# Kernel optimization log

Measured on AMD Instinct MI355X. Metric: run time of the kernel, lower is better.

Reference implementation:

```python
import jax, jax.numpy as jnp
import numpy as np

N, LQ, DM = 8, 2500, 256
NH, NL, NP, NZ = 8, 4, 8, 4
DH = DM // NH
SPATIAL = np.array([[64, 176], [32, 88], [16, 44], [8, 22]], dtype=np.int32)
LEN_IN = int((SPATIAL[:, 0] * SPATIAL[:, 1]).sum())


def setup_inputs() -> dict:
    key = jax.random.key(0)
    ks = jax.random.split(key, 10)
    query = jax.random.normal(ks[0], (N, LQ, DM), dtype=jnp.float32)
    query_pos = jax.random.normal(ks[1], (N, LQ, DM), dtype=jnp.float32)
    reference_points = jax.random.uniform(ks[2], (N, LQ, NZ, 2), dtype=jnp.float32)
    input_flatten = jax.random.normal(ks[3], (N, LEN_IN, DM), dtype=jnp.float32)
    input_spatial_shapes = jnp.asarray(SPATIAL)
    lsi = np.concatenate([[0], np.cumsum(SPATIAL[:, 0] * SPATIAL[:, 1])[:-1]]).astype(np.int32)
    input_level_start_index = jnp.asarray(lsi)
    # learned params (Linear: y = x @ W + b, W is (in, out))
    Wv = jax.random.normal(ks[4], (DM, DM), dtype=jnp.float32) * (1.0 / np.sqrt(DM))
    bv = jnp.zeros((DM,), dtype=jnp.float32)
    Wo = jax.random.normal(ks[5], (DM, NH * NL * NP * 2), dtype=jnp.float32) * 0.02
    bo = jax.random.normal(ks[6], (NH * NL * NP * 2,), dtype=jnp.float32) * 1.0
    Wa = jax.random.normal(ks[7], (DM, NH * NL * NP), dtype=jnp.float32) * 0.02
    ba = jnp.zeros((NH * NL * NP,), dtype=jnp.float32)
    return {"query": query, "query_pos": query_pos, "reference_points": reference_points,
            "input_flatten": input_flatten, "input_spatial_shapes": input_spatial_shapes,
            "input_level_start_index": input_level_start_index,
            "Wv": Wv, "bv": bv, "Wo": Wo, "bo": bo, "Wa": Wa, "ba": ba}


def _sample_level(v, h, w, loc):
    """Bilinear sample (grid_sample, align_corners=False, zero padding).
    v:   (N, h*w, NH, DH) level feature map
    loc: (N, Lq, NH, P, 2) normalized locations in [0,1] (x, y)
    returns (N, NH, Lq, P, DH)
    """
    n, hw, nh, dh = v.shape
    lq, p = loc.shape[1], loc.shape[3]
    x = loc[..., 0] * w - 0.5
    y = loc[..., 1] * h - 0.5
    x0f = jnp.floor(x)
    y0f = jnp.floor(y)
    wx = x - x0f
    wy = y - y0f
    x0 = x0f.astype(jnp.int32)
    y0 = y0f.astype(jnp.int32)
    vt = v.transpose(0, 2, 1, 3).reshape(n * nh, hw, dh)

    def gather(xi, yi, wgt):
        valid = ((xi >= 0) & (xi < w) & (yi >= 0) & (yi < h)).astype(v.dtype)
        idx = jnp.clip(yi, 0, h - 1) * w + jnp.clip(xi, 0, w - 1)  # (N,Lq,NH,P)
        idx = idx.transpose(0, 2, 1, 3).reshape(n * nh, lq * p)
        g = jnp.take_along_axis(vt, idx[:, :, None], axis=1)  # (N*NH, Lq*P, DH)
        wv = (wgt * valid).transpose(0, 2, 1, 3).reshape(n * nh, lq * p)
        return g * wv[:, :, None]

    out = (gather(x0, y0, (1 - wx) * (1 - wy))
           + gather(x0 + 1, y0, wx * (1 - wy))
           + gather(x0, y0 + 1, (1 - wx) * wy)
           + gather(x0 + 1, y0 + 1, wx * wy))
    return out.reshape(n, nh, lq, p, dh)


def _forward(query, query_pos, reference_points, input_flatten, spatial, Wv, bv, Wo, bo, Wa, ba):
    n, lq, _ = query.shape
    len_in = input_flatten.shape[1]
    # projections
    value = (input_flatten @ Wv + bv).reshape(n, len_in, NH, DH)
    off = (query @ Wo + bo).reshape(n, lq, NH, NL, NP, 2)
    aw = jax.nn.softmax((query @ Wa + ba).reshape(n, lq, NH, NL * NP), axis=-1)
    aw = aw.reshape(n, lq, NH, NL, NP)
    # normalize offsets by (W_l, H_l), add to Z-anchor reference points
    norm = jnp.asarray(np.stack([spatial[:, 1], spatial[:, 0]], -1), dtype=query.dtype)  # (NL,2)
    off = off / norm[None, None, None, :, None, :]
    off = off.reshape(n, lq, NH, NL, NP // NZ, NZ, 2)
    ref = reference_points[:, :, None, None, None, :, :]  # (N,Lq,1,1,1,NZ,2)
    loc = (ref + off).reshape(n, lq, NH, NL, NP, 2)
    # multi-scale deformable sampling + weighted reduction
    out = jnp.zeros((n, lq, NH, DH), dtype=query.dtype)
    start = 0
    for lvl in range(NL):
        h, w = int(spatial[lvl, 0]), int(spatial[lvl, 1])
        v_l = value[:, start:start + h * w]
        start += h * w
        samp = _sample_level(v_l, h, w, loc[:, :, :, lvl])  # (N,NH,Lq,NP,DH)
        out = out + jnp.einsum('nhqpd,nqhp->nqhd', samp, aw[:, :, :, lvl])
    return out.reshape(n, lq, DM)


def reference(query, query_pos, reference_points, input_flatten, input_spatial_shapes,
              input_level_start_index, Wv, bv, Wo, bo, Wa, ba):
    spatial = np.asarray(jax.device_get(input_spatial_shapes))
    return _forward(query, query_pos, reference_points, input_flatten, spatial,
                    Wv, bv, Wo, bo, Wa, ba)
```

## Files before the change

### kernel.cpp

```cpp
#include <hip/hip_runtime.h>
#include <hip/hip_fp16.h>

#define N_BATCH 8
#define LQ_     2500
#define DM_     256
#define NH_     8
#define NL_     4
#define NP_     8
#define DH_     32
#define LEN_IN_ 14960
#define KDIM    256

#define MV_   119680
#define MQ_   20000
#define NBMV  935
#define NBMQ  157
#define NVB   1872
#define NCB   960

__constant__ int c_w[4]     = {176, 88, 44, 22};
__constant__ int c_h[4]     = {64, 32, 16, 8};
__constant__ int c_start[4] = {0, 11264, 14080, 14784};

using bf16x8 = __attribute__((ext_vector_type(8))) short;
using f32x4  = __attribute__((ext_vector_type(4))) float;

#define GLDS16(g, l)                                                         \
    __builtin_amdgcn_global_load_lds(                                        \
        (const __attribute__((address_space(1))) void*)(g),                  \
        (__attribute__((address_space(3))) void*)(l), 16, 0, 0)

static __device__ inline float fdot2_u(unsigned int p, unsigned int w, float c) {
    float r;
    asm("v_dot2_f32_f16 %0, %1, %2, %3" : "=v"(r) : "v"(p), "v"(w), "v"(c));
    return r;
}

static __device__ inline void split_bf16(float v, unsigned short& hi, unsigned short& lo) {
    unsigned int u = __float_as_uint(v);
    hi = (unsigned short)(u >> 16);
    float hif = __uint_as_float(u & 0xFFFF0000u);
    float l = v - hif;
    lo = (unsigned short)(__float_as_uint(l) >> 16);
}

static __device__ inline unsigned short f2bf_rne(float v) {
    unsigned int u = __float_as_uint(v);
    u += 0x7FFFu + ((u >> 16) & 1u);
    return (unsigned short)(u >> 16);
}

static __device__ inline unsigned short f2h_rne(float v) {
    _Float16 h = (_Float16)v;
    return __builtin_bit_cast(unsigned short, h);
}

static __device__ inline ushort4 cvt4_rne(float4 v) {
    ushort4 h;
    h.x = f2bf_rne(v.x);
    h.y = f2bf_rne(v.y);
    h.z = f2bf_rne(v.z);
    h.w = f2bf_rne(v.w);
    return h;
}

__global__ __launch_bounds__(256) void prep(
    const float* __restrict__ Wv, const float* __restrict__ Wo,
    const float* __restrict__ Wa, const float* __restrict__ bo,
    const float* __restrict__ ba,
    const float* __restrict__ input_flatten, const float* __restrict__ query,
    unsigned short* __restrict__ Wv_hi, unsigned short* __restrict__ Wv_lo,
    unsigned short* __restrict__ Wc_hi, unsigned short* __restrict__ Wc_lo,
    float* __restrict__ bcomb,
    unsigned short* __restrict__ Abf_v, unsigned short* __restrict__ Abf_q)
{
    const int b = blockIdx.x, tid = threadIdx.x;
    if (b < 2048) {
        const float4* s = (const float4*)input_flatten;
        ushort4*      d = (ushort4*)Abf_v;
        const int n8 = MV_ * KDIM / 8, st = 2048 * 256;
        for (int i = b * 256 + tid; i < n8; i += st) {
            d[2 * i]     = cvt4_rne(s[2 * i]);
            d[2 * i + 1] = cvt4_rne(s[2 * i + 1]);
        }
    } else if (b < 2560) {
        const float4* s = (const float4*)query;
        ushort4*      d = (ushort4*)Abf_q;
        const int n8 = MQ_ * KDIM / 8, st = 512 * 256;
        for (int i = (b - 2048) * 256 + tid; i < n8; i += st) {
            d[2 * i]     = cvt4_rne(s[2 * i]);
            d[2 * i + 1] = cvt4_rne(s[2 * i + 1]);
        }
    } else {
        const int base = (b - 2560) * 256 + tid;
        for (int id = base; id < 262144; id += 131072) {
            if (id < 65536) {
                int n = id >> 8, k = id & 255;
                unsigned short h, l;
                split_bf16(Wv[k * 256 + n], h, l);
                Wv_hi[id] = h; Wv_lo[id] = l;
            } else {
                int id2 = id - 65536;
                int n = id2 >> 8, k = id2 & 255;
                float v = (n < 512) ? Wo[k * 512 + n] : Wa[k * 256 + (n - 512)];
                unsigned short h, l;
                split_bf16(v, h, l);
                Wc_hi[id2] = h; Wc_lo[id2] = l;
            }
        }
        if (base < 768) bcomb[base] = (base < 512) ? bo[base] : ba[base - 512];
    }
}

__global__ __launch_bounds__(512, 8) void gemm2(
    const unsigned short* __restrict__ Av,
    const unsigned short* __restrict__ Aq,
    const unsigned short* __restrict__ Wvh, const unsigned short* __restrict__ Wvl,
    const unsigned short* __restrict__ Wch, const unsigned short* __restrict__ Wcl,
    const float* __restrict__ bv, const float* __restrict__ bc,
    float* __restrict__ Cq,
    unsigned short* __restrict__ Cv)
{
    __shared__ __align__(16) unsigned short As [4096];
    __shared__ __align__(16) unsigned short Bhs[4096];
    __shared__ __align__(16) unsigned short Bls[4096];

    const int tid = threadIdx.x;
    const int bid = blockIdx.x;
    const bool is_comb = (bid >= NVB);

    const unsigned short *A, *Bth, *Btl;
    const float* bias;
    int by, bx, M, N;
    if (is_comb) {
        int cid = bid - NVB;
        int xcd = cid & 7, j = cid >> 3;
        by = xcd + 8 * (j / 6); bx = j % 6;
        if (by >= NBMQ) return;
        A = Aq; Bth = Wch; Btl = Wcl; bias = bc;
        M = MQ_; N = 768;
    } else {
        int xcd = bid & 7, j = bid >> 3;
        by = xcd + 8 * (j >> 1); bx = j & 1;
        if (by >= NBMV) return;
        A = Av; Bth = Wvh; Btl = Wvl; bias = bv;
        M = MV_; N = 256;
    }

    const int row0 = by << 7, col0 = bx << 7;
    const int lane = tid & 63, wave = tid >> 6;
    const int wrow = (wave & 1) << 6, wcol = (wave >> 1) << 5;
    const int r16  = lane & 15, quad = lane >> 4;

    const int srow = tid >> 2, skq = tid & 3;
    const int arow = min(row0 + srow, M - 1);
    const unsigned short* gA  = A   + (size_t)arow * KDIM + skq * 8;
    const unsigned short* gBh = Bth + (size_t)(col0 + srow) * KDIM + skq * 8;
    const unsigned short* gBl = Btl + (size_t)(col0 + srow) * KDIM + skq * 8;
    unsigned short* lA  = &As [wave << 9];
    unsigned short* lBh = &Bhs[wave << 9];
    unsigned short* lBl = &Bls[wave << 9];

    f32x4 acc[4][2];
#pragma unroll
    for (int i = 0; i < 4; ++i)
#pragma unroll
        for (int j = 0; j < 2; ++j) acc[i][j] = (f32x4){0.f, 0.f, 0.f, 0.f};

#pragma unroll
    for (int kt = 0; kt < 8; ++kt) {
        GLDS16(gA  + kt * 32, lA);
        GLDS16(gBh + kt * 32, lBh);
        GLDS16(gBl + kt * 32, lBl);
        __syncthreads();

        bf16x8 fbh[2], fbl[2], fa[4];
#pragma unroll
        for (int tn = 0; tn < 2; ++tn) {
            int n = wcol + tn * 16 + r16;
            fbh[tn] = *(const bf16x8*)&Bhs[n * 32 + (quad << 3)];
            fbl[tn] = *(const bf16x8*)&Bls[n * 32 + (quad << 3)];
        }
#pragma unroll
        for (int tm = 0; tm < 4; ++tm)
            fa[tm] = *(const bf16x8*)&As[(wrow + tm * 16 + r16) * 32 + (quad << 3)];
#pragma unroll
        for (int tm = 0; tm < 4; ++tm)
#pragma unroll
            for (int tn = 0; tn < 2; ++tn) {
                acc[tm][tn] = __builtin_amdgcn_mfma_f32_16x16x32_bf16(fa[tm], fbl[tn], acc[tm][tn], 0, 0, 0);
                acc[tm][tn] = __builtin_amdgcn_mfma_f32_16x16x32_bf16(fa[tm], fbh[tn], acc[tm][tn], 0, 0, 0);
            }
        __syncthreads();
    }

    float bvs[2];
#pragma unroll
    for (int tn = 0; tn < 2; ++tn) bvs[tn] = bias[col0 + wcol + tn * 16 + r16];
#pragma unroll
    for (int tm = 0; tm < 4; ++tm) {
#pragma unroll
        for (int i = 0; i < 4; ++i) {
            int row = row0 + wrow + tm * 16 + (quad << 2) + i;
            if (row < M) {
                if (is_comb) {
                    float* crow = Cq + (size_t)row * N + col0 + wcol + r16;
#pragma unroll
                    for (int tn = 0; tn < 2; ++tn)
                        crow[tn * 16] = acc[tm][tn][i] + bvs[tn];
                } else {
                    int n   = row / LEN_IN_;
                    int pix = row - n * LEN_IN_;
#pragma unroll
                    for (int tn = 0; tn < 2; ++tn) {
                        int col = col0 + wcol + tn * 16 + r16;
                        int h = col >> 5, dh = col & 31;
                        size_t addr = ((size_t)(n * NH_ + h) * LEN_IN_ + pix) * DH_ + dh;
                        Cv[addr] = f2h_rne(acc[tm][tn][i] + bvs[tn]);
                    }
                }
            }
        }
    }
}

__global__ __launch_bounds__(256, 4) void ms_sample(
    const unsigned short* __restrict__ value,
    const float* __restrict__ comb,
    const float* __restrict__ ref_pts,
    float* __restrict__ out)
{
    __shared__ uint4 s_desc[64][33];

    const int b     = blockIdx.x;
    const int xcd   = b & 7;
    const int j     = b >> 3;
    const int slice = (j / 40) * 8 + xcd;
    const int chunk = j % 40;
    const int n     = slice >> 3, h = slice & 7;
    const int q0    = chunk * 64;
    const int tid   = threadIdx.x;

    {
        int ql = tid >> 2, l = tid & 3;
        int q  = q0 + ql;
        if (q < LQ_) {
            int nq = n * LQ_ + q;
            const float* row = comb + (size_t)nq * 768;

            float4 L0 = *(const float4*)&row[512 + h * 32 + l * 8];
            float4 L1 = *(const float4*)&row[512 + h * 32 + l * 8 + 4];
            float lg[8] = {L0.x, L0.y, L0.z, L0.w, L1.x, L1.y, L1.z, L1.w};
            float m = lg[0];
#pragma unroll
            for (int i = 1; i < 8; ++i) m = fmaxf(m, lg[i]);
            m = fmaxf(m, __shfl_xor(m, 1));
            m = fmaxf(m, __shfl_xor(m, 2));
            float e[8], s = 0.f;
#pragma unroll
            for (int i = 0; i < 8; ++i) { e[i] = __expf(lg[i] - m); s += e[i]; }
            s += __shfl_xor(s, 1);
            s += __shfl_xor(s, 2);
            float inv = 1.f / s;

            float4 R0 = *(const float4*)&ref_pts[(size_t)nq * 8];
            float4 R1 = *(const float4*)&ref_pts[(size_t)nq * 8 + 4];
            float rx[4] = {R0.x, R0.z, R1.x, R1.z};
            float ry[4] = {R0.y, R0.w, R1.y, R1.w};

            float off[16];
#pragma unroll
            for (int i = 0; i < 4; ++i)
                *(float4*)&off[i * 4] = *(const float4*)&row[h * 64 + l * 16 + i * 4];

            float wl = (float)c_w[l], hl = (float)c_h[l];
            int wli = c_w[l], hli = c_h[l], st = c_start[l];
#pragma unroll
            for (int p = 0; p < 8; ++p) {
                int z = p & 3;
                float a = e[p] * inv;
                float x = rx[z] * wl + off[p * 2 + 0] - 0.5f;
                float y = ry[z] * hl + off[p * 2 + 1] - 0.5f;
                float x0f = floorf(x), y0f = floorf(y);
                int   x0 = (int)x0f,  y0 = (int)y0f;
                float wx = x - x0f,   wy = y - y0f;
                unsigned short ix[4];
                float wt[4];
#pragma unroll
                for (int jj = 0; jj < 4; ++jj) {
                    int xi = x0 + (jj & 1);
                    int yi = y0 + (jj >> 1);
                    float w = ((jj & 1) ? wx : 1.f - wx) * ((jj >> 1) ? wy : 1.f - wy);
                    bool valid = (xi >= 0) && (xi < wli) && (yi >= 0) && (yi < hli);
                    int xc = min(max(xi, 0), wli - 1);
                    int yc = min(max(yi, 0), hli - 1);
                    ix[jj] = (unsigned short)(yc * wli + xc);
                    wt[jj] = valid ? a * w : 0.f;
                }
                uint4 d;
                d.x = (unsigned int)(st + ix[0]) | ((unsigned int)(st + ix[1]) << 16);
                d.y = (unsigned int)(st + ix[2]) | ((unsigned int)(st + ix[3]) << 16);
                __half2 h01 = __floats2half2_rn(wt[0], wt[1]);
                __half2 h23 = __floats2half2_rn(wt[2], wt[3]);
                d.z = *(unsigned int*)&h01;
                d.w = *(unsigned int*)&h23;
                s_desc[ql][l * 8 + p] = d;
            }
        }
    }
    __syncthreads();

    int ql = tid >> 2, dhg = tid & 3;
    int q  = q0 + ql;
    if (q >= LQ_) return;
    int nq = n * LQ_ + q;
    const unsigned short* vb = value
        + ((size_t)(n * NH_ + h) * LEN_IN_) * DH_ + dhg * 8;

    float acc[8];
#pragma unroll
    for (int i = 0; i < 8; ++i) acc[i] = 0.f;

#pragma unroll 4
    for (int s = 0; s < 32; ++s) {
        uint4 d = s_desc[ql][s];
        int i0 = d.x & 0xFFFF, i1 = d.x >> 16;
        int i2 = d.y & 0xFFFF, i3 = d.y >> 16;
        uint4 v0 = *(const uint4*)(vb + i0 * DH_);
        uint4 v1 = *(const uint4*)(vb + i1 * DH_);
        uint4 v2 = *(const uint4*)(vb + i2 * DH_);
        uint4 v3 = *(const uint4*)(vb + i3 * DH_);
        acc[0] = fdot2_u(__builtin_amdgcn_perm(v1.x, v0.x, 0x05040100u), d.z, acc[0]);
        acc[1] = fdot2_u(__builtin_amdgcn_perm(v1.x, v0.x, 0x07060302u), d.z, acc[1]);
        acc[2] = fdot2_u(__builtin_amdgcn_perm(v1.y, v0.y, 0x05040100u), d.z, acc[2]);
        acc[3] = fdot2_u(__builtin_amdgcn_perm(v1.y, v0.y, 0x07060302u), d.z, acc[3]);
        acc[4] = fdot2_u(__builtin_amdgcn_perm(v1.z, v0.z, 0x05040100u), d.z, acc[4]);
        acc[5] = fdot2_u(__builtin_amdgcn_perm(v1.z, v0.z, 0x07060302u), d.z, acc[5]);
        acc[6] = fdot2_u(__builtin_amdgcn_perm(v1.w, v0.w, 0x05040100u), d.z, acc[6]);
        acc[7] = fdot2_u(__builtin_amdgcn_perm(v1.w, v0.w, 0x07060302u), d.z, acc[7]);
        acc[0] = fdot2_u(__builtin_amdgcn_perm(v3.x, v2.x, 0x05040100u), d.w, acc[0]);
        acc[1] = fdot2_u(__builtin_amdgcn_perm(v3.x, v2.x, 0x07060302u), d.w, acc[1]);
        acc[2] = fdot2_u(__builtin_amdgcn_perm(v3.y, v2.y, 0x05040100u), d.w, acc[2]);
        acc[3] = fdot2_u(__builtin_amdgcn_perm(v3.y, v2.y, 0x07060302u), d.w, acc[3]);
        acc[4] = fdot2_u(__builtin_amdgcn_perm(v3.z, v2.z, 0x05040100u), d.w, acc[4]);
        acc[5] = fdot2_u(__builtin_amdgcn_perm(v3.z, v2.z, 0x07060302u), d.w, acc[5]);
        acc[6] = fdot2_u(__builtin_amdgcn_perm(v3.w, v2.w, 0x05040100u), d.w, acc[6]);
        acc[7] = fdot2_u(__builtin_amdgcn_perm(v3.w, v2.w, 0x07060302u), d.w, acc[7]);
    }

    float* op = out + (size_t)nq * 256 + h * 32 + dhg * 8;
    *(float4*)&op[0] = make_float4(acc[0], acc[1], acc[2], acc[3]);
    *(float4*)&op[4] = make_float4(acc[4], acc[5], acc[6], acc[7]);
}

extern "C" void kernel_launch(void* const* d_in, const int* in_sizes, int n_in,
                              void* d_out, int out_size, void* d_ws, size_t ws_size,
                              hipStream_t stream)
{
    const float* query         = (const float*)d_in[0];
    const float* ref_pts       = (const float*)d_in[2];
    const float* input_flatten = (const float*)d_in[3];
    const float* Wv            = (const float*)d_in[6];
    const float* bv            = (const float*)d_in[7];
    const float* Wo            = (const float*)d_in[8];
    const float* bo            = (const float*)d_in[9];
    const float* Wa            = (const float*)d_in[10];
    const float* ba            = (const float*)d_in[11];
    float* out = (float*)d_out;

    char* ws = (char*)d_ws;
    size_t o = 0;
    unsigned short* Wv_hi = (unsigned short*)(ws + o); o += 256 * 256 * 2;
    unsigned short* Wv_lo = (unsigned short*)(ws + o); o += 256 * 256 * 2;
    unsigned short* Wc_hi = (unsigned short*)(ws + o); o += 768 * 256 * 2;
    unsigned short* Wc_lo = (unsigned short*)(ws + o); o += 768 * 256 * 2;
    float*          bcomb = (float*)(ws + o);          o += 768 * 4;
    o = (o + 511) & ~(size_t)511;
    unsigned short* value = (unsigned short*)(ws + o); o += (size_t)119680 * 256 * 2;
    o = (o + 511) & ~(size_t)511;
    float* combq = (float*)(ws + o); o += (size_t)20000 * 768 * 4;
    o = (o + 511) & ~(size_t)511;
    unsigned short* Abf_v = (unsigned short*)(ws + o); o += (size_t)MV_ * KDIM * 2;
    unsigned short* Abf_q = (unsigned short*)d_out;

    hipLaunchKernelGGL(prep, dim3(3072), dim3(256), 0, stream,
                       Wv, Wo, Wa, bo, ba, input_flatten, query,
                       Wv_hi, Wv_lo, Wc_hi, Wc_lo, bcomb, Abf_v, Abf_q);
    hipLaunchKernelGGL(gemm2, dim3(NVB + NCB), dim3(512), 0, stream,
                       Abf_v, Abf_q, Wv_hi, Wv_lo, Wc_hi, Wc_lo,
                       bv, bcomb, combq, value);
    hipLaunchKernelGGL(ms_sample, dim3(2560), dim3(256), 0, stream,
                       value, combq, ref_pts, out);
}
```

Baseline: 355.8 us.

## Fuse fp32-to-bf16 activation conversion into GEMM A-tile loading

Removes the separate prep pass that converted input_flatten and query to bf16 in a workspace buffer. The GEMM now loads fp32 A rows straight into registers, rounds them to bf16 and writes them to LDS, prefetching the next k-tile's A values after the barrier. This saves a full write and re-read of about 61MB of bf16 intermediate. In exchange the GEMM reads twice as many A bytes, uses more registers, and the A tile no longer uses the async global-to-LDS path.

```diff
diff --git a/kernel.cpp b/kernel.cpp
--- a/kernel.cpp
+++ b/kernel.cpp
@@ -55,66 +55,36 @@
     return __builtin_bit_cast(unsigned short, h);
 }
 
-static __device__ inline ushort4 cvt4_rne(float4 v) {
-    ushort4 h;
-    h.x = f2bf_rne(v.x);
-    h.y = f2bf_rne(v.y);
-    h.z = f2bf_rne(v.z);
-    h.w = f2bf_rne(v.w);
-    return h;
-}
-
-__global__ __launch_bounds__(256) void prep(
+__global__ __launch_bounds__(256) void conv_weights(
     const float* __restrict__ Wv, const float* __restrict__ Wo,
     const float* __restrict__ Wa, const float* __restrict__ bo,
     const float* __restrict__ ba,
-    const float* __restrict__ input_flatten, const float* __restrict__ query,
     unsigned short* __restrict__ Wv_hi, unsigned short* __restrict__ Wv_lo,
     unsigned short* __restrict__ Wc_hi, unsigned short* __restrict__ Wc_lo,
-    float* __restrict__ bcomb,
-    unsigned short* __restrict__ Abf_v, unsigned short* __restrict__ Abf_q)
+    float* __restrict__ bcomb)
 {
-    const int b = blockIdx.x, tid = threadIdx.x;
-    if (b < 2048) {
-        const float4* s = (const float4*)input_flatten;
-        ushort4*      d = (ushort4*)Abf_v;
-        const int n8 = MV_ * KDIM / 8, st = 2048 * 256;
-        for (int i = b * 256 + tid; i < n8; i += st) {
-            d[2 * i]     = cvt4_rne(s[2 * i]);
-            d[2 * i + 1] = cvt4_rne(s[2 * i + 1]);
-        }
-    } else if (b < 2560) {
-        const float4* s = (const float4*)query;
-        ushort4*      d = (ushort4*)Abf_q;
-        const int n8 = MQ_ * KDIM / 8, st = 512 * 256;
-        for (int i = (b - 2048) * 256 + tid; i < n8; i += st) {
-            d[2 * i]     = cvt4_rne(s[2 * i]);
-            d[2 * i + 1] = cvt4_rne(s[2 * i + 1]);
-        }
+    int id = blockIdx.x * 256 + threadIdx.x;
+    if (id < 256 * 256) {
+        int n = id >> 8, k = id & 255;
+        unsigned short h, l;
+        split_bf16(Wv[k * 256 + n], h, l);
+        Wv_hi[id] = h; Wv_lo[id] = l;
     } else {
-        const int base = (b - 2560) * 256 + tid;
-        for (int id = base; id < 262144; id += 131072) {
-            if (id < 65536) {
-                int n = id >> 8, k = id & 255;
-                unsigned short h, l;
-                split_bf16(Wv[k * 256 + n], h, l);
-                Wv_hi[id] = h; Wv_lo[id] = l;
-            } else {
-                int id2 = id - 65536;
-                int n = id2 >> 8, k = id2 & 255;
-                float v = (n < 512) ? Wo[k * 512 + n] : Wa[k * 256 + (n - 512)];
-                unsigned short h, l;
-                split_bf16(v, h, l);
-                Wc_hi[id2] = h; Wc_lo[id2] = l;
-            }
-        }
-        if (base < 768) bcomb[base] = (base < 512) ? bo[base] : ba[base - 512];
-    }
+        int id2 = id - 65536;
+        if (id2 < 768 * 256) {
+            int n = id2 >> 8, k = id2 & 255;
+            float v = (n < 512) ? Wo[k * 512 + n] : Wa[k * 256 + (n - 512)];
+            unsigned short h, l;
+            split_bf16(v, h, l);
+            Wc_hi[id2] = h; Wc_lo[id2] = l;
+        }
+    }
+    if (id < 768) bcomb[id] = (id < 512) ? bo[id] : ba[id - 512];
 }
 
 __global__ __launch_bounds__(512, 8) void gemm2(
-    const unsigned short* __restrict__ Av,
-    const unsigned short* __restrict__ Aq,
+    const float* __restrict__ Av,
+    const float* __restrict__ Aq,
     const unsigned short* __restrict__ Wvh, const unsigned short* __restrict__ Wvl,
     const unsigned short* __restrict__ Wch, const unsigned short* __restrict__ Wcl,
     const float* __restrict__ bv, const float* __restrict__ bc,
@@ -129,7 +99,8 @@
     const int bid = blockIdx.x;
     const bool is_comb = (bid >= NVB);
 
-    const unsigned short *A, *Bth, *Btl;
+    const float* A;
+    const unsigned short *Bth, *Btl;
     const float* bias;
     int by, bx, M, N;
     if (is_comb) {
@@ -154,12 +125,15 @@
 
     const int srow = tid >> 2, skq = tid & 3;
     const int arow = min(row0 + srow, M - 1);
-    const unsigned short* gA  = A   + (size_t)arow * KDIM + skq * 8;
+    const float* gA = A + (size_t)arow * KDIM + skq * 8;
     const unsigned short* gBh = Bth + (size_t)(col0 + srow) * KDIM + skq * 8;
     const unsigned short* gBl = Btl + (size_t)(col0 + srow) * KDIM + skq * 8;
-    unsigned short* lA  = &As [wave << 9];
     unsigned short* lBh = &Bhs[wave << 9];
     unsigned short* lBl = &Bls[wave << 9];
+    const int aoff = srow * 32 + skq * 8;
+
+    float4 a0 = *(const float4*)(gA + 0);
+    float4 a1 = *(const float4*)(gA + 4);
 
     f32x4 acc[4][2];
 #pragma unroll
@@ -169,10 +143,22 @@
 
 #pragma unroll
     for (int kt = 0; kt < 8; ++kt) {
-        GLDS16(gA  + kt * 32, lA);
         GLDS16(gBh + kt * 32, lBh);
         GLDS16(gBl + kt * 32, lBl);
+        {
+            bf16x8 hv;
+            hv[0] = (short)f2bf_rne(a0.x); hv[1] = (short)f2bf_rne(a0.y);
+            hv[2] = (short)f2bf_rne(a0.z); hv[3] = (short)f2bf_rne(a0.w);
+            hv[4] = (short)f2bf_rne(a1.x); hv[5] = (short)f2bf_rne(a1.y);
+            hv[6] = (short)f2bf_rne(a1.z); hv[7] = (short)f2bf_rne(a1.w);
+            *(bf16x8*)&As[aoff] = hv;
+        }
         __syncthreads();
+
+        if (kt < 7) {
+            a0 = *(const float4*)(gA + (kt + 1) * 32);
+            a1 = *(const float4*)(gA + (kt + 1) * 32 + 4);
+        }
 
         bf16x8 fbh[2], fbl[2], fa[4];
 #pragma unroll
@@ -379,15 +365,11 @@
     unsigned short* value = (unsigned short*)(ws + o); o += (size_t)119680 * 256 * 2;
     o = (o + 511) & ~(size_t)511;
     float* combq = (float*)(ws + o); o += (size_t)20000 * 768 * 4;
-    o = (o + 511) & ~(size_t)511;
-    unsigned short* Abf_v = (unsigned short*)(ws + o); o += (size_t)MV_ * KDIM * 2;
-    unsigned short* Abf_q = (unsigned short*)d_out;
-
-    hipLaunchKernelGGL(prep, dim3(3072), dim3(256), 0, stream,
-                       Wv, Wo, Wa, bo, ba, input_flatten, query,
-                       Wv_hi, Wv_lo, Wc_hi, Wc_lo, bcomb, Abf_v, Abf_q);
+
+    hipLaunchKernelGGL(conv_weights, dim3(1024), dim3(256), 0, stream,
+                       Wv, Wo, Wa, bo, ba, Wv_hi, Wv_lo, Wc_hi, Wc_lo, bcomb);
     hipLaunchKernelGGL(gemm2, dim3(NVB + NCB), dim3(512), 0, stream,
-                       Abf_v, Abf_q, Wv_hi, Wv_lo, Wc_hi, Wc_lo,
+                       input_flatten, query, Wv_hi, Wv_lo, Wc_hi, Wc_lo,
                        bv, bcomb, combq, value);
     hipLaunchKernelGGL(ms_sample, dim3(2560), dim3(256), 0, stream,
                        value, combq, ref_pts, out);
```

Measured after the change: 507.9 us. 42.7% more time.
